# Kernel optimization log

Hardware: AMD Instinct MI355X
Metric: run time of the kernel (lower is better)

## Reference

```python
import jax, jax.numpy as jnp
import numpy as np

N_NODES = 50000
N_EDGES = 800000
D = 96
H2 = 32
OUT = 4


def _glorot(key, shape):
    fan_in, fan_out = shape[0], shape[1]
    lim = (6.0 / (fan_in + fan_out)) ** 0.5
    return jax.random.uniform(key, shape, jnp.float32, -lim, lim)


def setup_inputs() -> dict:
    key = jax.random.key(0)
    ks = jax.random.split(key, 12)
    x = jax.random.normal(ks[0], (N_NODES, D), jnp.float32)
    edge_index = jax.random.randint(ks[1], (2, N_EDGES), 0, N_NODES, jnp.int32)
    return {
        "x": x,
        "edge_index": edge_index,
        "eps1": jnp.float32(0.0),
        "eps2": jnp.float32(0.0),
        "W1a": _glorot(ks[2], (D, D)),  "b1a": jnp.zeros((D,), jnp.float32),
        "W1b": _glorot(ks[3], (D, D)),  "b1b": jnp.zeros((D,), jnp.float32),
        "W2a": _glorot(ks[4], (D, H2)), "b2a": jnp.zeros((H2,), jnp.float32),
        "W2b": _glorot(ks[5], (H2, H2)),"b2b": jnp.zeros((H2,), jnp.float32),
        "Wh": _glorot(ks[6], (H2, OUT)),"bh": jnp.zeros((OUT,), jnp.float32),
    }


def _gin_agg(h, src, dst):
    # sum_{j in N(i)} h_j : gather source features, scatter-add to destination
    return jax.ops.segment_sum(h[src], dst, num_segments=N_NODES)


def reference(x, edge_index, eps1, eps2, W1a, b1a, W1b, b1b, W2a, b2a, W2b, b2b, Wh, bh):
    src, dst = edge_index[0], edge_index[1]

    # GIN layer 1: mlp1((1+eps1)*x + agg(x)), then outer ReLU (dropout is eval-mode identity)
    z = (1.0 + eps1) * x + _gin_agg(x, src, dst)           # [N, D]
    h = jax.nn.relu(z @ W1a + b1a) @ W1b + b1b             # mlp1
    h = jax.nn.relu(h)

    # GIN layer 2: mlp2((1+eps2)*h + agg(h)), then outer ReLU
    z2 = (1.0 + eps2) * h + _gin_agg(h, src, dst)          # [N, D]
    h2 = jax.nn.relu(z2 @ W2a + b2a) @ W2b + b2b           # mlp2 -> [N, 32]
    h2 = jax.nn.relu(h2)

    return h2 @ Wh + bh                                    # [N, 4]
```

## Files before the change

kernel.cpp:

```cpp
#include <hip/hip_runtime.h>

#define NN 50000
#define NE 800000
#define DD 96
#define HH 32
#define OO 4
#define ELLW 64
#define NBUCK 196
#define BCAP 8192

typedef unsigned short ushort_t;
typedef unsigned int uint_t;
typedef __attribute__((ext_vector_type(8))) short short8;
typedef __attribute__((ext_vector_type(4))) float f32x4;

__device__ inline ushort_t f2bf(float f) {
    uint_t b = __float_as_uint(f);
    return (ushort_t)((b + 0x7fffu + ((b >> 16) & 1u)) >> 16);
}

__device__ inline void addbf8(float* a, uint4 u) {
    a[0] += __uint_as_float(u.x << 16);
    a[1] += __uint_as_float(u.x & 0xffff0000u);
    a[2] += __uint_as_float(u.y << 16);
    a[3] += __uint_as_float(u.y & 0xffff0000u);
    a[4] += __uint_as_float(u.z << 16);
    a[5] += __uint_as_float(u.z & 0xffff0000u);
    a[6] += __uint_as_float(u.w << 16);
    a[7] += __uint_as_float(u.w & 0xffff0000u);
}


#define BA_B   196
#define WF_B   6

__global__ void k_pre(const int* __restrict__ edges, int* __restrict__ bcnt,
                      uint_t* __restrict__ packed,
                      const float* __restrict__ W1b, const float* __restrict__ W2a,
                      ushort_t* __restrict__ wf) {
    int b = blockIdx.x;
    if (b < BA_B) {
        __shared__ int hist[NBUCK];
        __shared__ int basesh[NBUCK];
        int thr = threadIdx.x;
        if (thr < NBUCK) hist[thr] = 0;
        __syncthreads();
#pragma unroll
        for (int k = 0; k < 4; ++k) {
            int t4 = b * 1024 + k * 256 + thr;
            if (t4 < NE / 4) {
                int4 tt = ((const int4*)(edges + NE))[t4];
                atomicAdd(&hist[tt.x >> 8], 1);
                atomicAdd(&hist[tt.y >> 8], 1);
                atomicAdd(&hist[tt.z >> 8], 1);
                atomicAdd(&hist[tt.w >> 8], 1);
            }
        }
        __syncthreads();
        if (thr < NBUCK) {
            int c = hist[thr];
            basesh[thr] = c ? atomicAdd(&bcnt[thr], c) : 0;
        }
        __syncthreads();
        if (thr < NBUCK) hist[thr] = 0;
        __syncthreads();
#pragma unroll
        for (int k = 0; k < 4; ++k) {
            int t4 = b * 1024 + k * 256 + thr;
            if (t4 < NE / 4) {
                int4 ss = ((const int4*)edges)[t4];
                int4 tt = ((const int4*)(edges + NE))[t4];
                int b0 = tt.x >> 8, b1 = tt.y >> 8, b2 = tt.z >> 8, b3 = tt.w >> 8;
                int p0 = basesh[b0] + atomicAdd(&hist[b0], 1);
                int p1 = basesh[b1] + atomicAdd(&hist[b1], 1);
                int p2 = basesh[b2] + atomicAdd(&hist[b2], 1);
                int p3 = basesh[b3] + atomicAdd(&hist[b3], 1);
                if (p0 < BCAP) packed[(size_t)b0 * BCAP + p0] = ((uint_t)ss.x << 8) | (tt.x & 255);
                if (p1 < BCAP) packed[(size_t)b1 * BCAP + p1] = ((uint_t)ss.y << 8) | (tt.y & 255);
                if (p2 < BCAP) packed[(size_t)b2 * BCAP + p2] = ((uint_t)ss.z << 8) | (tt.z & 255);
                if (p3 < BCAP) packed[(size_t)b3 * BCAP + p3] = ((uint_t)ss.w << 8) | (tt.w & 255);
            }
        }
        return;
    }
    b -= BA_B;
    int tw = b * 256 + threadIdx.x;
    if (tw < 1152 + 384) {
        const float* Wsrc; ushort_t* dst; int KOUT, fl;
        if (tw < 1152) { Wsrc = W1b; dst = wf;        KOUT = DD; fl = tw; }
        else           { Wsrc = W2a; dst = wf + 9216; KOUT = HH; fl = tw - 1152; }
        int lane = fl & 63;
        int fc = fl >> 6;
        int c = fc % 3, nt = fc / 3;
        int kb = c * 32 + (lane >> 4) * 8;
        int col = nt * 16 + (lane & 15);
        ushort_t v[8];
#pragma unroll
        for (int j = 0; j < 8; ++j)
            v[j] = f2bf(Wsrc[(size_t)(kb + j) * KOUT + col]);
        *(uint4*)(dst + (size_t)fl * 8) = *(uint4*)v;
    }
}


#define MT1    (NN / 16)
#define MFMA1_B ((MT1 + 3) / 4)

__global__ void k_main(const int* __restrict__ bcnt, const uint_t* __restrict__ packed,
                       ushort_t* __restrict__ ell, int* __restrict__ deg,
                       const float* __restrict__ x, const float* __restrict__ W1a,
                       ushort_t* __restrict__ y1) {
    __shared__ __align__(16) ushort_t lds[1152 * 8];
    int b = blockIdx.x;
    int thr = threadIdx.x;
    if (b < NBUCK) {
        int* curL = (int*)lds;
        int n0 = b * 256;
        curL[thr] = 0;
        __syncthreads();
        int cnt = min(bcnt[b], BCAP);
        const uint_t* pk = packed + (size_t)b * BCAP;
        for (int e = thr; e < cnt; e += 256) {
            uint_t u = pk[e];
            int doff = u & 255;
            int src = u >> 8;
            int p = atomicAdd(&curL[doff], 1);
            if (p < ELLW) ell[(size_t)(n0 + doff) * ELLW + p] = (ushort_t)src;
        }
        __syncthreads();
        if (n0 + thr < NN) deg[n0 + thr] = curL[thr];
        return;
    }
    b -= NBUCK;
    constexpr int KC = 3, NT = 6;
    for (int fl = thr; fl < 1152; fl += 256) {
        int lane_f = fl & 63;
        int fc = fl >> 6;
        int c = fc % 3, nt = fc / 3;
        int kb = c * 32 + (lane_f >> 4) * 8;
        int col = nt * 16 + (lane_f & 15);
        ushort_t v[8];
#pragma unroll
        for (int j = 0; j < 8; ++j)
            v[j] = f2bf(W1a[(size_t)(kb + j) * DD + col]);
        *(uint4*)(lds + (size_t)fl * 8) = *(uint4*)v;
    }
    __syncthreads();

    int lane = thr & 63;
    int widx = thr >> 6;
    int tile = b * 4 + widx;
    if (tile >= MT1) return;
    int row0 = tile * 16;
    int q = lane >> 4;
    int l16 = lane & 15;

    short8 bf[NT][KC];
#pragma unroll
    for (int nt = 0; nt < NT; ++nt)
#pragma unroll
        for (int c = 0; c < KC; ++c)
            bf[nt][c] = *(short8*)(lds + ((size_t)(nt * 3 + c) * 64 + lane) * 8);

    short8 af[KC];
#pragma unroll
    for (int c = 0; c < KC; ++c) {
        const float* ap = x + (size_t)(row0 + l16) * DD + c * 32 + q * 8;
        float4 f0 = *(const float4*)ap;
        float4 f1 = *(const float4*)(ap + 4);
        ushort_t v[8] = {f2bf(f0.x), f2bf(f0.y), f2bf(f0.z), f2bf(f0.w),
                         f2bf(f1.x), f2bf(f1.y), f2bf(f1.z), f2bf(f1.w)};
        af[c] = *(short8*)v;
    }

    f32x4 acc[NT];
#pragma unroll
    for (int nt = 0; nt < NT; ++nt) acc[nt] = (f32x4){0.f, 0.f, 0.f, 0.f};
#pragma unroll
    for (int nt = 0; nt < NT; ++nt)
#pragma unroll
        for (int c = 0; c < KC; ++c)
            acc[nt] = __builtin_amdgcn_mfma_f32_16x16x32_bf16(af[c], bf[nt][c], acc[nt], 0, 0, 0);

#pragma unroll
    for (int nt = 0; nt < NT; ++nt) {
        int s = nt >> 1;
        int c32 = (nt & 1) * 16 + l16;
#pragma unroll
        for (int r = 0; r < 4; ++r)
            y1[(size_t)s * NN * 32 + (size_t)(row0 + q * 4 + r) * 32 + c32] = f2bf(acc[nt][r]);
    }
}


__global__ void k_aggb96(const ushort_t* __restrict__ y, const int* __restrict__ deg,
                         const ushort_t* __restrict__ ell, const float* __restrict__ eps_p,
                         const float* __restrict__ b, ushort_t* __restrict__ out) {
    int idx = blockIdx.x * blockDim.x + threadIdx.x;
    if (idx >= NN * 24) return;
    int s = idx / (NN * 8);
    int rem = idx - s * (NN * 8);
    int i = rem >> 3;
    int sub = rem & 7;
    int v = sub >> 1, part = sub & 1;
    const uint4* ys = (const uint4*)(y + (size_t)s * NN * 32);
    const ushort_t* er = ell + (size_t)i * ELLW;
    int d = min(deg[i], ELLW);
    float a0[8] = {0,0,0,0,0,0,0,0}, a1[8] = {0,0,0,0,0,0,0,0};
    float a2[8] = {0,0,0,0,0,0,0,0}, a3[8] = {0,0,0,0,0,0,0,0};
    int p = part;
    for (; p + 6 < d; p += 8) {
        int s0 = er[p], s1 = er[p+2], s2 = er[p+4], s3 = er[p+6];
        uint4 f0 = ys[(size_t)s0 * 4 + v];
        uint4 f1 = ys[(size_t)s1 * 4 + v];
        uint4 f2 = ys[(size_t)s2 * 4 + v];
        uint4 f3 = ys[(size_t)s3 * 4 + v];
        addbf8(a0, f0); addbf8(a1, f1); addbf8(a2, f2); addbf8(a3, f3);
    }
    for (; p < d; p += 2) addbf8(a0, ys[(size_t)er[p] * 4 + v]);

    float sm[8];
#pragma unroll
    for (int k = 0; k < 8; ++k) {
        sm[k] = (a0[k] + a1[k]) + (a2[k] + a3[k]);
        sm[k] += __shfl_xor(sm[k], 1);
    }
    if (part) return;

    uint4 su = ys[(size_t)i * 4 + v];
    float s8[8];
    s8[0] = __uint_as_float(su.x << 16); s8[1] = __uint_as_float(su.x & 0xffff0000u);
    s8[2] = __uint_as_float(su.y << 16); s8[3] = __uint_as_float(su.y & 0xffff0000u);
    s8[4] = __uint_as_float(su.z << 16); s8[5] = __uint_as_float(su.z & 0xffff0000u);
    s8[6] = __uint_as_float(su.w << 16); s8[7] = __uint_as_float(su.w & 0xffff0000u);
    float4 bl = ((const float4*)b)[s * 8 + v * 2];
    float4 bhv = ((const float4*)b)[s * 8 + v * 2 + 1];
    float bb[8] = {bl.x, bl.y, bl.z, bl.w, bhv.x, bhv.y, bhv.z, bhv.w};
    float e = 1.0f + eps_p[0];
    ushort_t r[8];
#pragma unroll
    for (int k = 0; k < 8; ++k) {
        float vv = fmaf(e, s8[k], sm[k]) + bb[k];
        r[k] = f2bf(fmaxf(vv, 0.0f));
    }
    uint4 o;
    o.x = (uint_t)r[0] | ((uint_t)r[1] << 16);
    o.y = (uint_t)r[2] | ((uint_t)r[3] << 16);
    o.z = (uint_t)r[4] | ((uint_t)r[5] << 16);
    o.w = (uint_t)r[6] | ((uint_t)r[7] << 16);
    ((uint4*)out)[(size_t)i * 12 + s * 4 + v] = o;
}


#define HSTRIDE 104

__global__ void k_mfma23(const ushort_t* __restrict__ t1, const ushort_t* __restrict__ wf,
                         const float* __restrict__ b1b, ushort_t* __restrict__ y2) {
    constexpr int KC = 3, NT1 = 6, NT2 = 2;
    __shared__ __align__(16) ushort_t hT[4][16 * HSTRIDE];
    int lane = threadIdx.x & 63;
    int widx = threadIdx.x >> 6;
    int tile = blockIdx.x * 4 + widx;
    bool live = tile < MT1;
    int row0 = tile * 16;
    int q = lane >> 4;
    int l16 = lane & 15;
    const short8* bfp1 = (const short8*)wf;
    const short8* bfp2 = (const short8*)(wf + 9216);

    if (live) {
        short8 bf[NT1][KC];
#pragma unroll
        for (int nt = 0; nt < NT1; ++nt)
#pragma unroll
            for (int c = 0; c < KC; ++c)
                bf[nt][c] = bfp1[(nt * KC + c) * 64 + lane];

        short8 af[KC];
#pragma unroll
        for (int c = 0; c < KC; ++c) {
            uint4 av = *(const uint4*)(t1 + (size_t)(row0 + l16) * DD + c * 32 + q * 8);
            af[c] = *(short8*)&av;
        }

        f32x4 acc[NT1];
#pragma unroll
        for (int nt = 0; nt < NT1; ++nt) acc[nt] = (f32x4){0.f, 0.f, 0.f, 0.f};
#pragma unroll
        for (int nt = 0; nt < NT1; ++nt)
#pragma unroll
            for (int c = 0; c < KC; ++c)
                acc[nt] = __builtin_amdgcn_mfma_f32_16x16x32_bf16(af[c], bf[nt][c], acc[nt], 0, 0, 0);

#pragma unroll
        for (int nt = 0; nt < NT1; ++nt) {
            int col = nt * 16 + l16;
            float bv = b1b[col];
#pragma unroll
            for (int r = 0; r < 4; ++r)
                hT[widx][(q * 4 + r) * HSTRIDE + col] = f2bf(fmaxf(acc[nt][r] + bv, 0.0f));
        }
    }
    __syncthreads();
    if (!live) return;

    short8 af2[KC];
#pragma unroll
    for (int c = 0; c < KC; ++c) {
        uint4 av = *(const uint4*)&hT[widx][l16 * HSTRIDE + c * 32 + q * 8];
        af2[c] = *(short8*)&av;
    }
    short8 bf2[NT2][KC];
#pragma unroll
    for (int nt = 0; nt < NT2; ++nt)
#pragma unroll
        for (int c = 0; c < KC; ++c)
            bf2[nt][c] = bfp2[(nt * KC + c) * 64 + lane];

    f32x4 acc2[NT2];
#pragma unroll
    for (int nt = 0; nt < NT2; ++nt) acc2[nt] = (f32x4){0.f, 0.f, 0.f, 0.f};
#pragma unroll
    for (int nt = 0; nt < NT2; ++nt)
#pragma unroll
        for (int c = 0; c < KC; ++c)
            acc2[nt] = __builtin_amdgcn_mfma_f32_16x16x32_bf16(af2[c], bf2[nt][c], acc2[nt], 0, 0, 0);

#pragma unroll
    for (int nt = 0; nt < NT2; ++nt) {
        int col = nt * 16 + l16;
#pragma unroll
        for (int r = 0; r < 4; ++r)
            y2[(size_t)(row0 + q * 4 + r) * HH + col] = f2bf(acc2[nt][r]);
    }
}


#define TSTRIDE 36
#define ATR 16

__global__ void k_aggtail(const ushort_t* __restrict__ y2, const int* __restrict__ deg,
                          const ushort_t* __restrict__ ell, const float* __restrict__ eps_p,
                          const float* __restrict__ b2a, const float* __restrict__ W2b,
                          const float* __restrict__ b2b, const float* __restrict__ Wh,
                          const float* __restrict__ bhp, float* __restrict__ out) {
    __shared__ float t2f[ATR * TSTRIDE];
    int row = threadIdx.x >> 4;
    int sub = threadIdx.x & 15;
    int jg = sub & 3;
    int part = sub >> 2;
    int i = blockIdx.x * ATR + row;
    bool live = i < NN;

    if (live) {
        const uint4* y4 = (const uint4*)y2;
        const ushort_t* er = ell + (size_t)i * ELLW;
        int d = min(deg[i], ELLW);
        float a0[8] = {0,0,0,0,0,0,0,0}, a1[8] = {0,0,0,0,0,0,0,0};
        int p = part;
        for (; p + 4 < d; p += 8) {
            int s0 = er[p], s1 = er[p + 4];
            uint4 f0 = y4[(size_t)s0 * 4 + jg];
            uint4 f1 = y4[(size_t)s1 * 4 + jg];
            addbf8(a0, f0); addbf8(a1, f1);
        }
        for (; p < d; p += 4) addbf8(a0, y4[(size_t)er[p] * 4 + jg]);

        float s[8];
#pragma unroll
        for (int k = 0; k < 8; ++k) {
            s[k] = a0[k] + a1[k];
            s[k] += __shfl_xor(s[k], 4);
            s[k] += __shfl_xor(s[k], 8);
        }
        if (part == 0) {
            uint4 su = y4[(size_t)i * 4 + jg];
            float s8[8];
            s8[0] = __uint_as_float(su.x << 16); s8[1] = __uint_as_float(su.x & 0xffff0000u);
            s8[2] = __uint_as_float(su.y << 16); s8[3] = __uint_as_float(su.y & 0xffff0000u);
            s8[4] = __uint_as_float(su.z << 16); s8[5] = __uint_as_float(su.z & 0xffff0000u);
            s8[6] = __uint_as_float(su.w << 16); s8[7] = __uint_as_float(su.w & 0xffff0000u);
            float4 bl = ((const float4*)b2a)[2 * jg];
            float4 bhv = ((const float4*)b2a)[2 * jg + 1];
            float bb[8] = {bl.x, bl.y, bl.z, bl.w, bhv.x, bhv.y, bhv.z, bhv.w};
            float e = 1.0f + eps_p[0];
#pragma unroll
            for (int k = 0; k < 8; ++k) {
                float vv = fmaf(e, s8[k], s[k]) + bb[k];
                t2f[row * TSTRIDE + jg * 8 + k] = fmaxf(vv, 0.0f);
            }
        }
    }
    __syncthreads();

    float o[OO] = {0.f, 0.f, 0.f, 0.f};
    if (live) {
        const float* tr = &t2f[row * TSTRIDE];
#pragma unroll
        for (int jj = 0; jj < 2; ++jj) {
            int j = sub * 2 + jj;
            float acc = b2b[j];
#pragma unroll 8
            for (int k = 0; k < HH; ++k)
                acc = fmaf(tr[k], W2b[k * HH + j], acc);
            acc = fmaxf(acc, 0.0f);
#pragma unroll
            for (int oo = 0; oo < OO; ++oo)
                o[oo] = fmaf(acc, Wh[j * OO + oo], o[oo]);
        }
    }
#pragma unroll
    for (int oo = 0; oo < OO; ++oo) {
        o[oo] += __shfl_xor(o[oo], 1);
        o[oo] += __shfl_xor(o[oo], 2);
        o[oo] += __shfl_xor(o[oo], 4);
        o[oo] += __shfl_xor(o[oo], 8);
    }
    if (live && sub == 0) {
        float4 ov = {o[0] + bhp[0], o[1] + bhp[1], o[2] + bhp[2], o[3] + bhp[3]};
        ((float4*)out)[i] = ov;
    }
}


extern "C" void kernel_launch(void* const* d_in, const int* in_sizes, int n_in,
                              void* d_out, int out_size, void* d_ws, size_t ws_size,
                              hipStream_t stream) {
    const float* x    = (const float*)d_in[0];
    const int*   edges= (const int*)d_in[1];
    const float* eps1 = (const float*)d_in[2];
    const float* eps2 = (const float*)d_in[3];
    const float* W1a  = (const float*)d_in[4];
    const float* b1a  = (const float*)d_in[5];
    const float* W1b  = (const float*)d_in[6];
    const float* b1b  = (const float*)d_in[7];
    const float* W2a  = (const float*)d_in[8];
    const float* b2a  = (const float*)d_in[9];
    const float* W2b  = (const float*)d_in[10];
    const float* b2b  = (const float*)d_in[11];
    const float* Wh   = (const float*)d_in[12];
    const float* bh   = (const float*)d_in[13];

    auto al = [](size_t n) { return (n + 255) / 256 * 256; };
    char* w = (char*)d_ws;
    int*      bcnt   = (int*)w;      w += al((size_t)NBUCK * 4);
    uint_t*   packed = (uint_t*)w;   w += al((size_t)NBUCK * BCAP * 4);
    int*      deg    = (int*)w;      w += al((size_t)NN * 4);
    ushort_t* ell    = (ushort_t*)w; w += al((size_t)NN * ELLW * 2);
    ushort_t* wf     = (ushort_t*)w; w += al((size_t)(9216 + 3072) * 2);
    ushort_t* y1     = (ushort_t*)w; w += al((size_t)NN * DD * 2);
    ushort_t* t1     = (ushort_t*)w; w += al((size_t)NN * DD * 2);
    ushort_t* y2     = (ushort_t*)w; w += al((size_t)NN * HH * 2);

    const int B = 256;

    hipMemsetAsync(bcnt, 0, (size_t)NBUCK * 4, stream);
    k_pre<<<BA_B + WF_B, B, 0, stream>>>(edges, bcnt, packed, W1b, W2a, wf);
    k_main<<<NBUCK + MFMA1_B, B, 0, stream>>>(bcnt, packed, ell, deg, x, W1a, y1);
    k_aggb96<<<(NN * 24 + B - 1) / B, B, 0, stream>>>(y1, deg, ell, eps1, b1a, t1);
    k_mfma23<<<MFMA1_B, B, 0, stream>>>(t1, wf, b1b, y2);
    k_aggtail<<<(NN + ATR - 1) / ATR, B, 0, stream>>>(y2, deg, ell, eps2, b2a, W2b, b2b,
                                                      Wh, bh, (float*)d_out);
}
```

Baseline: 181.8 us.

## Build ELL adjacency directly with global atomics and merge preprocessing kernels

Drops the two-pass bucketed counting sort (per-block histogram, packed bucket array, then per-bucket LDS scatter) and instead builds the ELL adjacency directly with one global atomicAdd on deg per edge. The edge scatter, weight-fragment conversion and the first MFMA GEMM now share a single launch, removing one kernel launch and the packed intermediate buffer. The cost is 800K global atomics spread over 50K counters instead of LDS atomics, and ELL writes that are more scattered.

```diff
diff --git a/kernel.cpp b/kernel.cpp
--- a/kernel.cpp
+++ b/kernel.cpp
@@ -6,8 +6,6 @@
 #define HH 32
 #define OO 4
 #define ELLW 64
-#define NBUCK 196
-#define BCAP 8192
 
 typedef unsigned short ushort_t;
 typedef unsigned int uint_t;
@@ -31,107 +29,63 @@
 }
 
 
-#define BA_B   196
+#define EDGE_B 196
 #define WF_B   6
-
-__global__ void k_pre(const int* __restrict__ edges, int* __restrict__ bcnt,
-                      uint_t* __restrict__ packed,
-                      const float* __restrict__ W1b, const float* __restrict__ W2a,
-                      ushort_t* __restrict__ wf) {
+#define MT1    (NN / 16)
+#define MFMA1_B ((MT1 + 3) / 4)
+
+__global__ void k_fused1(const int* __restrict__ edges, int* __restrict__ deg,
+                         ushort_t* __restrict__ ell,
+                         const float* __restrict__ W1b, const float* __restrict__ W2a,
+                         ushort_t* __restrict__ wf,
+                         const float* __restrict__ x, const float* __restrict__ W1a,
+                         ushort_t* __restrict__ y1) {
+    __shared__ __align__(16) ushort_t lds[1152 * 8];
     int b = blockIdx.x;
-    if (b < BA_B) {
-        __shared__ int hist[NBUCK];
-        __shared__ int basesh[NBUCK];
-        int thr = threadIdx.x;
-        if (thr < NBUCK) hist[thr] = 0;
-        __syncthreads();
-#pragma unroll
-        for (int k = 0; k < 4; ++k) {
-            int t4 = b * 1024 + k * 256 + thr;
-            if (t4 < NE / 4) {
-                int4 tt = ((const int4*)(edges + NE))[t4];
-                atomicAdd(&hist[tt.x >> 8], 1);
-                atomicAdd(&hist[tt.y >> 8], 1);
-                atomicAdd(&hist[tt.z >> 8], 1);
-                atomicAdd(&hist[tt.w >> 8], 1);
-            }
-        }
-        __syncthreads();
-        if (thr < NBUCK) {
-            int c = hist[thr];
-            basesh[thr] = c ? atomicAdd(&bcnt[thr], c) : 0;
-        }
-        __syncthreads();
-        if (thr < NBUCK) hist[thr] = 0;
-        __syncthreads();
+    int thr = threadIdx.x;
+
+    if (b < EDGE_B) {
 #pragma unroll
         for (int k = 0; k < 4; ++k) {
             int t4 = b * 1024 + k * 256 + thr;
             if (t4 < NE / 4) {
                 int4 ss = ((const int4*)edges)[t4];
                 int4 tt = ((const int4*)(edges + NE))[t4];
-                int b0 = tt.x >> 8, b1 = tt.y >> 8, b2 = tt.z >> 8, b3 = tt.w >> 8;
-                int p0 = basesh[b0] + atomicAdd(&hist[b0], 1);
-                int p1 = basesh[b1] + atomicAdd(&hist[b1], 1);
-                int p2 = basesh[b2] + atomicAdd(&hist[b2], 1);
-                int p3 = basesh[b3] + atomicAdd(&hist[b3], 1);
-                if (p0 < BCAP) packed[(size_t)b0 * BCAP + p0] = ((uint_t)ss.x << 8) | (tt.x & 255);
-                if (p1 < BCAP) packed[(size_t)b1 * BCAP + p1] = ((uint_t)ss.y << 8) | (tt.y & 255);
-                if (p2 < BCAP) packed[(size_t)b2 * BCAP + p2] = ((uint_t)ss.z << 8) | (tt.z & 255);
-                if (p3 < BCAP) packed[(size_t)b3 * BCAP + p3] = ((uint_t)ss.w << 8) | (tt.w & 255);
+                int p0 = atomicAdd(&deg[tt.x], 1);
+                int p1 = atomicAdd(&deg[tt.y], 1);
+                int p2 = atomicAdd(&deg[tt.z], 1);
+                int p3 = atomicAdd(&deg[tt.w], 1);
+                if (p0 < ELLW) ell[(size_t)tt.x * ELLW + p0] = (ushort_t)ss.x;
+                if (p1 < ELLW) ell[(size_t)tt.y * ELLW + p1] = (ushort_t)ss.y;
+                if (p2 < ELLW) ell[(size_t)tt.z * ELLW + p2] = (ushort_t)ss.z;
+                if (p3 < ELLW) ell[(size_t)tt.w * ELLW + p3] = (ushort_t)ss.w;
             }
         }
         return;
     }
-    b -= BA_B;
-    int tw = b * 256 + threadIdx.x;
-    if (tw < 1152 + 384) {
-        const float* Wsrc; ushort_t* dst; int KOUT, fl;
-        if (tw < 1152) { Wsrc = W1b; dst = wf;        KOUT = DD; fl = tw; }
-        else           { Wsrc = W2a; dst = wf + 9216; KOUT = HH; fl = tw - 1152; }
-        int lane = fl & 63;
-        int fc = fl >> 6;
-        int c = fc % 3, nt = fc / 3;
-        int kb = c * 32 + (lane >> 4) * 8;
-        int col = nt * 16 + (lane & 15);
-        ushort_t v[8];
-#pragma unroll
-        for (int j = 0; j < 8; ++j)
-            v[j] = f2bf(Wsrc[(size_t)(kb + j) * KOUT + col]);
-        *(uint4*)(dst + (size_t)fl * 8) = *(uint4*)v;
-    }
-}
-
-
-#define MT1    (NN / 16)
-#define MFMA1_B ((MT1 + 3) / 4)
-
-__global__ void k_main(const int* __restrict__ bcnt, const uint_t* __restrict__ packed,
-                       ushort_t* __restrict__ ell, int* __restrict__ deg,
-                       const float* __restrict__ x, const float* __restrict__ W1a,
-                       ushort_t* __restrict__ y1) {
-    __shared__ __align__(16) ushort_t lds[1152 * 8];
-    int b = blockIdx.x;
-    int thr = threadIdx.x;
-    if (b < NBUCK) {
-        int* curL = (int*)lds;
-        int n0 = b * 256;
-        curL[thr] = 0;
-        __syncthreads();
-        int cnt = min(bcnt[b], BCAP);
-        const uint_t* pk = packed + (size_t)b * BCAP;
-        for (int e = thr; e < cnt; e += 256) {
-            uint_t u = pk[e];
-            int doff = u & 255;
-            int src = u >> 8;
-            int p = atomicAdd(&curL[doff], 1);
-            if (p < ELLW) ell[(size_t)(n0 + doff) * ELLW + p] = (ushort_t)src;
-        }
-        __syncthreads();
-        if (n0 + thr < NN) deg[n0 + thr] = curL[thr];
+    b -= EDGE_B;
+
+    if (b < WF_B) {
+        int tw = b * 256 + thr;
+        if (tw < 1152 + 384) {
+            const float* Wsrc; ushort_t* dst; int KOUT, fl;
+            if (tw < 1152) { Wsrc = W1b; dst = wf;        KOUT = DD; fl = tw; }
+            else           { Wsrc = W2a; dst = wf + 9216; KOUT = HH; fl = tw - 1152; }
+            int lane = fl & 63;
+            int fc = fl >> 6;
+            int c = fc % 3, nt = fc / 3;
+            int kb = c * 32 + (lane >> 4) * 8;
+            int col = nt * 16 + (lane & 15);
+            ushort_t v[8];
+#pragma unroll
+            for (int j = 0; j < 8; ++j)
+                v[j] = f2bf(Wsrc[(size_t)(kb + j) * KOUT + col]);
+            *(uint4*)(dst + (size_t)fl * 8) = *(uint4*)v;
+        }
         return;
     }
-    b -= NBUCK;
+    b -= WF_B;
+
     constexpr int KC = 3, NT = 6;
     for (int fl = thr; fl < 1152; fl += 256) {
         int lane_f = fl & 63;
@@ -443,8 +397,6 @@
 
     auto al = [](size_t n) { return (n + 255) / 256 * 256; };
     char* w = (char*)d_ws;
-    int*      bcnt   = (int*)w;      w += al((size_t)NBUCK * 4);
-    uint_t*   packed = (uint_t*)w;   w += al((size_t)NBUCK * BCAP * 4);
     int*      deg    = (int*)w;      w += al((size_t)NN * 4);
     ushort_t* ell    = (ushort_t*)w; w += al((size_t)NN * ELLW * 2);
     ushort_t* wf     = (ushort_t*)w; w += al((size_t)(9216 + 3072) * 2);
@@ -454,9 +406,9 @@
 
     const int B = 256;
 
-    hipMemsetAsync(bcnt, 0, (size_t)NBUCK * 4, stream);
-    k_pre<<<BA_B + WF_B, B, 0, stream>>>(edges, bcnt, packed, W1b, W2a, wf);
-    k_main<<<NBUCK + MFMA1_B, B, 0, stream>>>(bcnt, packed, ell, deg, x, W1a, y1);
+    hipMemsetAsync(deg, 0, (size_t)NN * 4, stream);
+    k_fused1<<<EDGE_B + WF_B + MFMA1_B, B, 0, stream>>>(edges, deg, ell, W1b, W2a, wf,
+                                                        x, W1a, y1);
     k_aggb96<<<(NN * 24 + B - 1) / B, B, 0, stream>>>(y1, deg, ell, eps1, b1a, t1);
     k_mfma23<<<MFMA1_B, B, 0, stream>>>(t1, wf, b1b, y2);
     k_aggtail<<<(NN + ATR - 1) / ATR, B, 0, stream>>>(y2, deg, ell, eps2, b2a, W2b, b2b,
```

Result: slower. 201.0 us (+10.6%).

## Fuse layer-1 gather aggregation into the following MFMA kernel via shared memory

Applied to the files above, without the earlier changes.

Merges the bf16 neighbour aggregation (k_aggb96) into the MFMA kernel that applies W1b and W2a. Each block first aggregates 64 nodes into LDS and then runs both matrix multiplies from LDS. This removes the t1 intermediate round-trip through global memory and one kernel launch. In exchange, the gather parallelism changes from 8 threads per node per slice to 4 threads per node covering all three slices, which lowers memory-level parallelism and occupancy during the latency-bound gather.

```diff
diff --git a/kernel.cpp b/kernel.cpp
--- a/kernel.cpp
+++ b/kernel.cpp
@@ -193,122 +193,122 @@
 }
 
 
-__global__ void k_aggb96(const ushort_t* __restrict__ y, const int* __restrict__ deg,
-                         const ushort_t* __restrict__ ell, const float* __restrict__ eps_p,
-                         const float* __restrict__ b, ushort_t* __restrict__ out) {
-    int idx = blockIdx.x * blockDim.x + threadIdx.x;
-    if (idx >= NN * 24) return;
-    int s = idx / (NN * 8);
-    int rem = idx - s * (NN * 8);
-    int i = rem >> 3;
-    int sub = rem & 7;
-    int v = sub >> 1, part = sub & 1;
-    const uint4* ys = (const uint4*)(y + (size_t)s * NN * 32);
-    const ushort_t* er = ell + (size_t)i * ELLW;
-    int d = min(deg[i], ELLW);
-    float a0[8] = {0,0,0,0,0,0,0,0}, a1[8] = {0,0,0,0,0,0,0,0};
-    float a2[8] = {0,0,0,0,0,0,0,0}, a3[8] = {0,0,0,0,0,0,0,0};
-    int p = part;
-    for (; p + 6 < d; p += 8) {
-        int s0 = er[p], s1 = er[p+2], s2 = er[p+4], s3 = er[p+6];
-        uint4 f0 = ys[(size_t)s0 * 4 + v];
-        uint4 f1 = ys[(size_t)s1 * 4 + v];
-        uint4 f2 = ys[(size_t)s2 * 4 + v];
-        uint4 f3 = ys[(size_t)s3 * 4 + v];
-        addbf8(a0, f0); addbf8(a1, f1); addbf8(a2, f2); addbf8(a3, f3);
-    }
-    for (; p < d; p += 2) addbf8(a0, ys[(size_t)er[p] * 4 + v]);
-
-    float sm[8];
-#pragma unroll
-    for (int k = 0; k < 8; ++k) {
-        sm[k] = (a0[k] + a1[k]) + (a2[k] + a3[k]);
-        sm[k] += __shfl_xor(sm[k], 1);
-    }
-    if (part) return;
-
-    uint4 su = ys[(size_t)i * 4 + v];
-    float s8[8];
-    s8[0] = __uint_as_float(su.x << 16); s8[1] = __uint_as_float(su.x & 0xffff0000u);
-    s8[2] = __uint_as_float(su.y << 16); s8[3] = __uint_as_float(su.y & 0xffff0000u);
-    s8[4] = __uint_as_float(su.z << 16); s8[5] = __uint_as_float(su.z & 0xffff0000u);
-    s8[6] = __uint_as_float(su.w << 16); s8[7] = __uint_as_float(su.w & 0xffff0000u);
-    float4 bl = ((const float4*)b)[s * 8 + v * 2];
-    float4 bhv = ((const float4*)b)[s * 8 + v * 2 + 1];
-    float bb[8] = {bl.x, bl.y, bl.z, bl.w, bhv.x, bhv.y, bhv.z, bhv.w};
-    float e = 1.0f + eps_p[0];
-    ushort_t r[8];
-#pragma unroll
-    for (int k = 0; k < 8; ++k) {
-        float vv = fmaf(e, s8[k], sm[k]) + bb[k];
-        r[k] = f2bf(fmaxf(vv, 0.0f));
-    }
-    uint4 o;
-    o.x = (uint_t)r[0] | ((uint_t)r[1] << 16);
-    o.y = (uint_t)r[2] | ((uint_t)r[3] << 16);
-    o.z = (uint_t)r[4] | ((uint_t)r[5] << 16);
-    o.w = (uint_t)r[6] | ((uint_t)r[7] << 16);
-    ((uint4*)out)[(size_t)i * 12 + s * 4 + v] = o;
-}
-
-
 #define HSTRIDE 104
 
-__global__ void k_mfma23(const ushort_t* __restrict__ t1, const ushort_t* __restrict__ wf,
-                         const float* __restrict__ b1b, ushort_t* __restrict__ y2) {
+__global__ void k_aggmm(const ushort_t* __restrict__ y1, const int* __restrict__ deg,
+                        const ushort_t* __restrict__ ell, const float* __restrict__ eps_p,
+                        const float* __restrict__ b1a, const ushort_t* __restrict__ wf,
+                        const float* __restrict__ b1b, ushort_t* __restrict__ y2) {
     constexpr int KC = 3, NT1 = 6, NT2 = 2;
-    __shared__ __align__(16) ushort_t hT[4][16 * HSTRIDE];
-    int lane = threadIdx.x & 63;
-    int widx = threadIdx.x >> 6;
+    __shared__ __align__(16) ushort_t hT[64 * HSTRIDE];
+    int thr = threadIdx.x;
+    int g = thr >> 2;
+    int u = thr & 3;
+    int i = blockIdx.x * 64 + g;
+    const uint4* ys0 = (const uint4*)y1;
+    const uint4* ys1 = (const uint4*)(y1 + (size_t)NN * 32);
+    const uint4* ys2 = (const uint4*)(y1 + (size_t)2 * NN * 32);
+
+    if (i < NN) {
+        const ushort_t* er = ell + (size_t)i * ELLW;
+        int d = min(deg[i], ELLW);
+        float a0[8] = {0,0,0,0,0,0,0,0}, a1[8] = {0,0,0,0,0,0,0,0}, a2[8] = {0,0,0,0,0,0,0,0};
+        float a3[8] = {0,0,0,0,0,0,0,0}, a4[8] = {0,0,0,0,0,0,0,0}, a5[8] = {0,0,0,0,0,0,0,0};
+        int p = 0;
+        for (; p + 1 < d; p += 2) {
+            int s0 = er[p], s1 = er[p + 1];
+            uint4 f00 = ys0[(size_t)s0 * 4 + u];
+            uint4 f10 = ys1[(size_t)s0 * 4 + u];
+            uint4 f20 = ys2[(size_t)s0 * 4 + u];
+            uint4 f01 = ys0[(size_t)s1 * 4 + u];
+            uint4 f11 = ys1[(size_t)s1 * 4 + u];
+            uint4 f21 = ys2[(size_t)s1 * 4 + u];
+            addbf8(a0, f00); addbf8(a1, f10); addbf8(a2, f20);
+            addbf8(a3, f01); addbf8(a4, f11); addbf8(a5, f21);
+        }
+        if (p < d) {
+            int s0 = er[p];
+            addbf8(a0, ys0[(size_t)s0 * 4 + u]);
+            addbf8(a1, ys1[(size_t)s0 * 4 + u]);
+            addbf8(a2, ys2[(size_t)s0 * 4 + u]);
+        }
+        float e = 1.0f + eps_p[0];
+        const float4* b4 = (const float4*)b1a;
+        ushort_t* dstg = &hT[g * HSTRIDE + u * 8];
+#pragma unroll
+        for (int s = 0; s < 3; ++s) {
+            const uint4* ysS = (s == 0) ? ys0 : (s == 1) ? ys1 : ys2;
+            const float* aa  = (s == 0) ? a0 : (s == 1) ? a1 : a2;
+            const float* ab  = (s == 0) ? a3 : (s == 1) ? a4 : a5;
+            uint4 su = ysS[(size_t)i * 4 + u];
+            float s8[8];
+            s8[0] = __uint_as_float(su.x << 16); s8[1] = __uint_as_float(su.x & 0xffff0000u);
+            s8[2] = __uint_as_float(su.y << 16); s8[3] = __uint_as_float(su.y & 0xffff0000u);
+            s8[4] = __uint_as_float(su.z << 16); s8[5] = __uint_as_float(su.z & 0xffff0000u);
+            s8[6] = __uint_as_float(su.w << 16); s8[7] = __uint_as_float(su.w & 0xffff0000u);
+            float4 bl = b4[s * 8 + u * 2];
+            float4 bh = b4[s * 8 + u * 2 + 1];
+            float bb[8] = {bl.x, bl.y, bl.z, bl.w, bh.x, bh.y, bh.z, bh.w};
+            ushort_t r[8];
+#pragma unroll
+            for (int k = 0; k < 8; ++k) {
+                float vv = fmaf(e, s8[k], aa[k] + ab[k]) + bb[k];
+                r[k] = f2bf(fmaxf(vv, 0.0f));
+            }
+            *(uint4*)(dstg + s * 32) = *(uint4*)r;
+        }
+    }
+    __syncthreads();
+
+    int lane = thr & 63;
+    int widx = thr >> 6;
     int tile = blockIdx.x * 4 + widx;
-    bool live = tile < MT1;
+    if (tile >= MT1) return;
     int row0 = tile * 16;
     int q = lane >> 4;
     int l16 = lane & 15;
     const short8* bfp1 = (const short8*)wf;
     const short8* bfp2 = (const short8*)(wf + 9216);
 
-    if (live) {
-        short8 bf[NT1][KC];
-#pragma unroll
-        for (int nt = 0; nt < NT1; ++nt)
-#pragma unroll
-            for (int c = 0; c < KC; ++c)
-                bf[nt][c] = bfp1[(nt * KC + c) * 64 + lane];
-
-        short8 af[KC];
-#pragma unroll
-        for (int c = 0; c < KC; ++c) {
-            uint4 av = *(const uint4*)(t1 + (size_t)(row0 + l16) * DD + c * 32 + q * 8);
-            af[c] = *(short8*)&av;
-        }
-
-        f32x4 acc[NT1];
-#pragma unroll
-        for (int nt = 0; nt < NT1; ++nt) acc[nt] = (f32x4){0.f, 0.f, 0.f, 0.f};
-#pragma unroll
-        for (int nt = 0; nt < NT1; ++nt)
-#pragma unroll
-            for (int c = 0; c < KC; ++c)
-                acc[nt] = __builtin_amdgcn_mfma_f32_16x16x32_bf16(af[c], bf[nt][c], acc[nt], 0, 0, 0);
-
-#pragma unroll
-        for (int nt = 0; nt < NT1; ++nt) {
-            int col = nt * 16 + l16;
-            float bv = b1b[col];
-#pragma unroll
-            for (int r = 0; r < 4; ++r)
-                hT[widx][(q * 4 + r) * HSTRIDE + col] = f2bf(fmaxf(acc[nt][r] + bv, 0.0f));
-        }
-    }
+    short8 bf[NT1][KC];
+#pragma unroll
+    for (int nt = 0; nt < NT1; ++nt)
+#pragma unroll
+        for (int c = 0; c < KC; ++c)
+            bf[nt][c] = bfp1[(nt * KC + c) * 64 + lane];
+
+    short8 af2[KC];
+#pragma unroll
+    for (int c = 0; c < KC; ++c) {
+        uint4 av = *(const uint4*)&hT[(widx * 16 + l16) * HSTRIDE + c * 32 + q * 8];
+        af2[c] = *(short8*)&av;
+    }
+
+    f32x4 acc[NT1];
+#pragma unroll
+    for (int nt = 0; nt < NT1; ++nt) acc[nt] = (f32x4){0.f, 0.f, 0.f, 0.f};
+#pragma unroll
+    for (int nt = 0; nt < NT1; ++nt)
+#pragma unroll
+        for (int c = 0; c < KC; ++c)
+            acc[nt] = __builtin_amdgcn_mfma_f32_16x16x32_bf16(af2[c], bf[nt][c], acc[nt], 0, 0, 0);
+
     __syncthreads();
-    if (!live) return;
-
-    short8 af2[KC];
+#pragma unroll
+    for (int nt = 0; nt < NT1; ++nt) {
+        int col = nt * 16 + l16;
+        float bv = b1b[col];
+#pragma unroll
+        for (int r = 0; r < 4; ++r)
+            hT[(widx * 16 + q * 4 + r) * HSTRIDE + col] = f2bf(fmaxf(acc[nt][r] + bv, 0.0f));
+    }
+    __syncthreads();
+
+    short8 af3[KC];
 #pragma unroll
     for (int c = 0; c < KC; ++c) {
-        uint4 av = *(const uint4*)&hT[widx][l16 * HSTRIDE + c * 32 + q * 8];
-        af2[c] = *(short8*)&av;
+        uint4 av = *(const uint4*)&hT[(widx * 16 + l16) * HSTRIDE + c * 32 + q * 8];
+        af3[c] = *(short8*)&av;
     }
     short8 bf2[NT2][KC];
 #pragma unroll
@@ -324,7 +324,7 @@
     for (int nt = 0; nt < NT2; ++nt)
 #pragma unroll
         for (int c = 0; c < KC; ++c)
-            acc2[nt] = __builtin_amdgcn_mfma_f32_16x16x32_bf16(af2[c], bf2[nt][c], acc2[nt], 0, 0, 0);
+            acc2[nt] = __builtin_amdgcn_mfma_f32_16x16x32_bf16(af3[c], bf2[nt][c], acc2[nt], 0, 0, 0);
 
 #pragma unroll
     for (int nt = 0; nt < NT2; ++nt) {
@@ -449,7 +449,6 @@
     ushort_t* ell    = (ushort_t*)w; w += al((size_t)NN * ELLW * 2);
     ushort_t* wf     = (ushort_t*)w; w += al((size_t)(9216 + 3072) * 2);
     ushort_t* y1     = (ushort_t*)w; w += al((size_t)NN * DD * 2);
-    ushort_t* t1     = (ushort_t*)w; w += al((size_t)NN * DD * 2);
     ushort_t* y2     = (ushort_t*)w; w += al((size_t)NN * HH * 2);
 
     const int B = 256;
@@ -457,8 +456,7 @@
     hipMemsetAsync(bcnt, 0, (size_t)NBUCK * 4, stream);
     k_pre<<<BA_B + WF_B, B, 0, stream>>>(edges, bcnt, packed, W1b, W2a, wf);
     k_main<<<NBUCK + MFMA1_B, B, 0, stream>>>(bcnt, packed, ell, deg, x, W1a, y1);
-    k_aggb96<<<(NN * 24 + B - 1) / B, B, 0, stream>>>(y1, deg, ell, eps1, b1a, t1);
-    k_mfma23<<<MFMA1_B, B, 0, stream>>>(t1, wf, b1b, y2);
+    k_aggmm<<<MFMA1_B, B, 0, stream>>>(y1, deg, ell, eps1, b1a, wf, b1b, y2);
     k_aggtail<<<(NN + ATR - 1) / ATR, B, 0, stream>>>(y2, deg, ell, eps2, b2a, W2b, b2b,
                                                       Wh, bh, (float*)d_out);
 }
```

After: 189.7 us. 4.3% more time.
